# Kernel tuning notes

Hardware: AMD Instinct MI355X
Metric: run time of the kernel (lower is better)

The kernel has to match this reference:

```python
import jax, jax.numpy as jnp
import numpy as np

EPS = 1e-5  # matches repo calc_mean_std eps


def _mvn(x):
    # mean-variance normalization per (B, C) over spatial dims, unbiased var (torch default)
    B, C, H, W = x.shape
    xf = x.reshape(B, C, H * W)
    m = xf.mean(-1, keepdims=True)
    v = xf.var(-1, ddof=1, keepdims=True)
    return ((xf - m) / jnp.sqrt(v + EPS)).reshape(x.shape)


def _conv1x1(x, w, b):
    # 1x1 conv == per-pixel channel mixing
    return jnp.einsum('oc,bchw->bohw', w, x) + b[None, :, None, None]


def _content_sa(x, Wp, bp):
    B, C, H, W = x.shape
    n = H * W
    xn = _mvn(x)
    q = _conv1x1(xn, Wp[0], bp[0]).reshape(B, C, n)  # f
    k = _conv1x1(xn, Wp[1], bp[1]).reshape(B, C, n)  # g
    energy = jnp.einsum('bci,bcj->bij', q, k)        # [B, N, N]
    attn = jax.nn.softmax(energy, axis=-1)
    v = _conv1x1(x, Wp[2], bp[2]).reshape(B, C, n)   # h
    out = jnp.einsum('bcj,bij->bci', v, attn).reshape(B, C, H, W)
    return _conv1x1(out, Wp[3], bp[3]) + x


def _style_sa(x, Wp, bp):
    B, C, H, W = x.shape
    n = H * W
    f = _conv1x1(x, Wp[0], bp[0]).reshape(B, C, n)
    g = _conv1x1(x, Wp[1], bp[1]).reshape(B, C, n)
    energy = jnp.einsum('bci,bdi->bcd', f, g)        # [B, C, C] channel attention
    attn = jax.nn.softmax(energy, axis=-1)
    h = _conv1x1(_mvn(x), Wp[2], bp[2]).reshape(B, C, n)
    out = jnp.einsum('bdc,bdi->bci', attn, h).reshape(B, C, H, W)  # attn^T @ h
    return _conv1x1(out, Wp[3], bp[3]) + x


def _ca(c, s, Wp, bp):
    B, C, Hc, Wc = c.shape
    nc = Hc * Wc
    _, _, Hs, Ws = s.shape
    ns = Hs * Ws
    q = _conv1x1(_mvn(c), Wp[0], bp[0]).reshape(B, C, nc)
    k = _conv1x1(_mvn(s), Wp[1], bp[1]).reshape(B, C, ns)
    energy = jnp.einsum('bci,bcj->bij', q, k)        # [B, Nc, Ns]
    attn = jax.nn.softmax(energy, axis=-1)
    v = _conv1x1(s, Wp[2], bp[2]).reshape(B, C, ns)
    out = jnp.einsum('bcj,bij->bci', v, attn).reshape(B, C, Hc, Wc)
    return _conv1x1(out, Wp[3], bp[3]) + c


def setup_inputs() -> dict:
    key = jax.random.key(0)
    ks = jax.random.split(key, 8)
    B, C, H, W = 4, 512, 64, 64
    scale = 0.02
    return {
        'content_feat': jax.random.normal(ks[0], (B, C, H, W), jnp.float32),
        'style_feat': jax.random.normal(ks[1], (B, C, H, W), jnp.float32),
        'csa_w': jax.random.normal(ks[2], (4, C, C), jnp.float32) * scale,
        'csa_b': jnp.zeros((4, C), jnp.float32),
        'ssa_w': jax.random.normal(ks[3], (4, C, C), jnp.float32) * scale,
        'ssa_b': jnp.zeros((4, C), jnp.float32),
        'ca_w': jax.random.normal(ks[4], (4, C, C), jnp.float32) * scale,
        'ca_b': jnp.zeros((4, C), jnp.float32),
    }


def reference(content_feat, style_feat, csa_w, csa_b, ssa_w, ssa_b, ca_w, ca_b):
    cf = _content_sa(content_feat, csa_w, csa_b)
    sf = _style_sa(style_feat, ssa_w, ssa_b)
    return _ca(cf, sf, ca_w, ca_b)
```

## Files before the change

### kernel.cpp

```cpp
#include <hip/hip_runtime.h>
#include <math.h>


#define B_ 4
#define C_ 512
#define N_ 4096
#define TM 128
#define TN 128

typedef unsigned short u16;
typedef __attribute__((ext_vector_type(8))) short s8v;
typedef __attribute__((ext_vector_type(4))) float f4v;

__device__ __forceinline__ u16 f2bf(float x) {
  unsigned u = __float_as_uint(x);
  return (u16)((u + 0x7fffu + ((u >> 16) & 1u)) >> 16);
}
__device__ __forceinline__ float bf2f(u16 h) {
  return __uint_as_float(((unsigned)h) << 16);
}
__device__ __forceinline__ u16 f2h(float x) {
  union { _Float16 h; u16 u; } z;
  z.h = (_Float16)x;
  return z.u;
}
__device__ __forceinline__ float h2f(u16 v) {
  union { _Float16 h; u16 u; } z;
  z.u = v;
  return (float)z.h;
}

__device__ __forceinline__ void gload16(const void* g, void* l) {
  __builtin_amdgcn_global_load_lds(
      (const __attribute__((address_space(1))) unsigned int*)g,
      (__attribute__((address_space(3))) unsigned int*)l, 16, 0, 0);
}

__device__ __forceinline__ float wave_red_sum(float v) {
#pragma unroll
  for (int off = 32; off > 0; off >>= 1) v += __shfl_xor(v, off, 64);
  return v;
}
__device__ __forceinline__ float wave_red_max(float v) {
#pragma unroll
  for (int off = 32; off > 0; off >>= 1) v = fmaxf(v, __shfl_xor(v, off, 64));
  return v;
}

__global__ __launch_bounds__(256) void row_stats_k(const float* __restrict__ x,
                                                   float* __restrict__ mean,
                                                   float* __restrict__ rstd) {
  long row = blockIdx.x;
  const float* p = x + row * (long)N_;
  int t = threadIdx.x;
  float s = 0.f, ss = 0.f;
  for (int i = t * 4; i < N_; i += 1024) {
    float4 v = *(const float4*)(p + i);
    s += v.x + v.y + v.z + v.w;
    ss += v.x * v.x + v.y * v.y + v.z * v.z + v.w * v.w;
  }
  __shared__ float rs_[4], rss_[4];
  int wid = t >> 6, lane = t & 63;
  s = wave_red_sum(s);
  ss = wave_red_sum(ss);
  if (lane == 0) { rs_[wid] = s; rss_[wid] = ss; }
  __syncthreads();
  if (t == 0) {
    float S = rs_[0] + rs_[1] + rs_[2] + rs_[3];
    float SS = rss_[0] + rss_[1] + rss_[2] + rss_[3];
    float m = S / (float)N_;
    float var = (SS - (float)N_ * m * m) / (float)(N_ - 1);
    mean[row] = m;
    rstd[row] = rsqrtf(var + 1e-5f);
  }
}

__global__ __launch_bounds__(256) void row_stats_bf_k(
    const u16* __restrict__ x, float* __restrict__ mean,
    float* __restrict__ rstd) {
  long row = blockIdx.x;
  const u16* p = x + row * (long)N_;
  int t = threadIdx.x;
  float s = 0.f, ss = 0.f;
  for (int i = t * 8; i < N_; i += 2048) {
    ushort4 a = *(const ushort4*)(p + i);
    ushort4 b = *(const ushort4*)(p + i + 4);
    float v0 = bf2f(a.x), v1 = bf2f(a.y), v2 = bf2f(a.z), v3 = bf2f(a.w);
    float v4 = bf2f(b.x), v5 = bf2f(b.y), v6 = bf2f(b.z), v7 = bf2f(b.w);
    s += v0 + v1 + v2 + v3 + v4 + v5 + v6 + v7;
    ss += v0 * v0 + v1 * v1 + v2 * v2 + v3 * v3 + v4 * v4 + v5 * v5 +
          v6 * v6 + v7 * v7;
  }
  __shared__ float rs_[4], rss_[4];
  int wid = t >> 6, lane = t & 63;
  s = wave_red_sum(s);
  ss = wave_red_sum(ss);
  if (lane == 0) { rs_[wid] = s; rss_[wid] = ss; }
  __syncthreads();
  if (t == 0) {
    float S = rs_[0] + rs_[1] + rs_[2] + rs_[3];
    float SS = rss_[0] + rss_[1] + rss_[2] + rss_[3];
    float m = S / (float)N_;
    float var = (SS - (float)N_ * m * m) / (float)(N_ - 1);
    mean[row] = m;
    rstd[row] = rsqrtf(var + 1e-5f);
  }
}

__global__ __launch_bounds__(256) void cvt3_k(
    const float* __restrict__ a, const float* __restrict__ b,
    const float* __restrict__ c, u16* __restrict__ oa, u16* __restrict__ ob,
    u16* __restrict__ oc, long n) {
  const float* in = blockIdx.y == 0 ? a : (blockIdx.y == 1 ? b : c);
  u16* o = blockIdx.y == 0 ? oa : (blockIdx.y == 1 ? ob : oc);
  long i = ((long)blockIdx.x * 256 + threadIdx.x) * 4;
  if (i >= n) return;
  float4 v = *(const float4*)(in + i);
  *(ushort4*)(o + i) = make_ushort4(f2bf(v.x), f2bf(v.y), f2bf(v.z), f2bf(v.w));
}

template <bool HAS2, bool HAS3>
__global__ __launch_bounds__(256) void t_cvt_k(
    const float* __restrict__ X, const float* __restrict__ mean,
    const float* __restrict__ rstd, u16* __restrict__ o1,
    u16* __restrict__ o2, u16* __restrict__ o3) {
  __shared__ float tile[64][68];
  const int b = blockIdx.z;
  const int c0 = blockIdx.y * 64, i0 = blockIdx.x * 64;
  const int t = threadIdx.x;
  const int tr = t >> 4, tc = (t & 15) << 2;
  const long CN = (long)C_ * N_;
  const float* Xb = X + (long)b * CN;
#pragma unroll
  for (int p2 = 0; p2 < 4; ++p2) {
    int c = p2 * 16 + tr;
    float4 v = *(const float4*)(Xb + (long)(c0 + c) * N_ + i0 + tc);
    tile[c][tc] = v.x;
    tile[c][tc + 1] = v.y;
    tile[c][tc + 2] = v.z;
    tile[c][tc + 3] = v.w;
    if (HAS3) {
      *(ushort4*)(o3 + (long)b * CN + (long)(c0 + c) * N_ + i0 + tc) =
          make_ushort4(f2bf(v.x), f2bf(v.y), f2bf(v.z), f2bf(v.w));
    }
  }
  __syncthreads();
  float mv[4], rv[4];
#pragma unroll
  for (int j = 0; j < 4; ++j) {
    mv[j] = mean[b * C_ + c0 + tc + j];
    rv[j] = rstd[b * C_ + c0 + tc + j];
  }
#pragma unroll
  for (int p2 = 0; p2 < 4; ++p2) {
    int ir = p2 * 16 + tr;
    long off = (long)b * CN + (long)(i0 + ir) * C_ + c0 + tc;
    u16 h1[4], h2[4];
#pragma unroll
    for (int j = 0; j < 4; ++j) {
      float v = tile[tc + j][ir];
      if (HAS2) h2[j] = f2bf(v);
      h1[j] = f2bf((v - mv[j]) * rv[j]);
    }
    *(ushort4*)(o1 + off) = make_ushort4(h1[0], h1[1], h1[2], h1[3]);
    if (HAS2) *(ushort4*)(o2 + off) = make_ushort4(h2[0], h2[1], h2[2], h2[3]);
  }
}

template <bool HAS2>
__global__ __launch_bounds__(256) void t_cvt_bf_k(
    const u16* __restrict__ X, const float* __restrict__ mean,
    const float* __restrict__ rstd, u16* __restrict__ o1,
    u16* __restrict__ o2) {
  __shared__ float tile[64][68];
  const int b = blockIdx.z;
  const int c0 = blockIdx.y * 64, i0 = blockIdx.x * 64;
  const int t = threadIdx.x;
  const int tr = t >> 4, tc = (t & 15) << 2;
  const long CN = (long)C_ * N_;
  const u16* Xb = X + (long)b * CN;
#pragma unroll
  for (int p2 = 0; p2 < 4; ++p2) {
    int c = p2 * 16 + tr;
    ushort4 v = *(const ushort4*)(Xb + (long)(c0 + c) * N_ + i0 + tc);
    tile[c][tc] = bf2f(v.x);
    tile[c][tc + 1] = bf2f(v.y);
    tile[c][tc + 2] = bf2f(v.z);
    tile[c][tc + 3] = bf2f(v.w);
  }
  __syncthreads();
  float mv[4], rv[4];
#pragma unroll
  for (int j = 0; j < 4; ++j) {
    mv[j] = mean[b * C_ + c0 + tc + j];
    rv[j] = rstd[b * C_ + c0 + tc + j];
  }
#pragma unroll
  for (int p2 = 0; p2 < 4; ++p2) {
    int ir = p2 * 16 + tr;
    long off = (long)b * CN + (long)(i0 + ir) * C_ + c0 + tc;
    u16 h1[4], h2[4];
#pragma unroll
    for (int j = 0; j < 4; ++j) {
      float v = tile[tc + j][ir];
      if (HAS2) h2[j] = f2bf(v);
      h1[j] = f2bf((v - mv[j]) * rv[j]);
    }
    *(ushort4*)(o1 + off) = make_ushort4(h1[0], h1[1], h1[2], h1[3]);
    if (HAS2) *(ushort4*)(o2 + off) = make_ushort4(h2[0], h2[1], h2[2], h2[3]);
  }
}

__global__ __launch_bounds__(256) void softmax_bf_k(const u16* __restrict__ E,
                                                    u16* __restrict__ ph) {
  long row = blockIdx.x;
  const u16* p = E + row * (long)N_;
  int t = threadIdx.x;
  float v[16];
  float mx = -3.4e38f;
#pragma unroll
  for (int q = 0; q < 4; ++q) {
    ushort4 w4 = *(const ushort4*)(p + t * 16 + q * 4);
    v[q * 4 + 0] = h2f(w4.x);
    v[q * 4 + 1] = h2f(w4.y);
    v[q * 4 + 2] = h2f(w4.z);
    v[q * 4 + 3] = h2f(w4.w);
    mx = fmaxf(mx, fmaxf(fmaxf(v[q * 4], v[q * 4 + 1]),
                         fmaxf(v[q * 4 + 2], v[q * 4 + 3])));
  }
  __shared__ float red[4];
  int wid = t >> 6, lane = t & 63;
  mx = wave_red_max(mx);
  if (lane == 0) red[wid] = mx;
  __syncthreads();
  mx = fmaxf(fmaxf(red[0], red[1]), fmaxf(red[2], red[3]));
  float s = 0.f;
#pragma unroll
  for (int i = 0; i < 16; ++i) {
    v[i] = __expf(v[i] - mx);
    s += v[i];
  }
  __syncthreads();
  s = wave_red_sum(s);
  if (lane == 0) red[wid] = s;
  __syncthreads();
  s = red[0] + red[1] + red[2] + red[3];
  float inv = 1.f / s;
  long ob = row * (long)N_ + t * 16;
#pragma unroll
  for (int q = 0; q < 4; ++q) {
    *(ushort4*)(ph + ob + q * 4) =
        make_ushort4(f2bf(v[q * 4 + 0] * inv), f2bf(v[q * 4 + 1] * inv),
                     f2bf(v[q * 4 + 2] * inv), f2bf(v[q * 4 + 3] * inv));
  }
}

__global__ __launch_bounds__(256) void softmax_t_k(const float* __restrict__ E2,
                                                   u16* __restrict__ ph) {
  int b = blockIdx.x >> 9;
  int x = blockIdx.x & 511;
  const float* p = E2 + ((long)b * C_ + x) * C_;
  int t = threadIdx.x;
  float v0 = p[t * 2], v1 = p[t * 2 + 1];
  float mx = fmaxf(v0, v1);
  __shared__ float red[4];
  int wid = t >> 6, lane = t & 63;
  mx = wave_red_max(mx);
  if (lane == 0) red[wid] = mx;
  __syncthreads();
  mx = fmaxf(fmaxf(red[0], red[1]), fmaxf(red[2], red[3]));
  v0 = __expf(v0 - mx);
  v1 = __expf(v1 - mx);
  float s = v0 + v1;
  __syncthreads();
  s = wave_red_sum(s);
  if (lane == 0) red[wid] = s;
  __syncthreads();
  s = red[0] + red[1] + red[2] + red[3];
  float inv = 1.f / s;
  long base = (long)b * C_ * C_;
  ph[base + (long)(t * 2) * C_ + x] = f2bf(v0 * inv);
  ph[base + (long)(t * 2 + 1) * C_ + x] = f2bf(v1 * inv);
}

__global__ __launch_bounds__(256) void redk_k(const float* __restrict__ P,
                                              long pKS, long perB, int nsplit,
                                              float* __restrict__ of,
                                              long total) {
  long e = ((long)blockIdx.x * 256 + threadIdx.x) * 4;
  if (e >= total) return;
  long b = e / perB, rem = e - b * perB;
  const float* p0 = P + b * perB + rem;
  float4 s = *(const float4*)p0;
  for (int k = 1; k < nsplit; ++k) {
    float4 t = *(const float4*)(p0 + (long)k * pKS);
    s.x += t.x;
    s.y += t.y;
    s.z += t.z;
    s.w += t.w;
  }
  *(float4*)(of + b * perB + rem) = s;
}

template <int OUTM, int BIAS, int RESM, bool SWAP>
__global__ __launch_bounds__(256, 3) void mm_k(
    const u16* __restrict__ Ap, long aBS, int lda,
    const u16* __restrict__ Bp, long bBS, int ldb,
    float* Of, u16* __restrict__ Obf, long oBS, long oKS, int ldo,
    const float* __restrict__ bias, const float* resp,
    const u16* __restrict__ res16, long rBS, int K, int nsplit) {
  __shared__ u16 lds[16384];
  const int bxi = SWAP ? blockIdx.y : blockIdx.x;
  const int byi = SWAP ? blockIdx.x : blockIdx.y;
  const int b = blockIdx.z / nsplit;
  const int ks = blockIdx.z % nsplit;
  const int Kc = K / nsplit;
  const int k0beg = ks * Kc;
  const int m0 = byi * TM, n0 = bxi * TN;
  const int t = threadIdx.x, lane = t & 63, wid = t >> 6;
  const int wm = (wid >> 1) * 64, wn = (wid & 1) * 64;

  const u16* srcp = (wid < 2) ? (Ap + (long)b * aBS) : (Bp + (long)b * bBS);
  const int sld = (wid < 2) ? lda : ldb;
  const long srow0 = ((wid < 2) ? m0 : n0) + (wid & 1) * 64;
  u16* dstb = &lds[wid * 4096];
  const int srg = lane >> 3;
  const int ssl = lane & 7;

  f4v acc[4][4];
#pragma unroll
  for (int i = 0; i < 4; ++i)
#pragma unroll
    for (int j = 0; j < 4; ++j) acc[i][j] = (f4v){0.f, 0.f, 0.f, 0.f};

  const int lr = lane & 15, ksl = lane >> 4;
  const u16* lA = &lds[0];
  const u16* lB = &lds[8192];

  for (int k0 = k0beg; k0 < k0beg + Kc; k0 += 64) {
#pragma unroll
    for (int s = 0; s < 8; ++s) {
      int r = s * 8 + srg;
      int kb = ((ssl ^ (r & 7)) << 4);
      const u16* gp = srcp + (srow0 + r) * (long)sld + k0;
      gload16((const char*)gp + kb, dstb + s * 512);
    }
    __syncthreads();
#pragma unroll
    for (int kk = 0; kk < 2; ++kk) {
      s8v ar[4], br[4];
#pragma unroll
      for (int f = 0; f < 4; ++f) {
        int ra = wm + f * 16 + lr;
        ar[f] = *(const s8v*)(lA + ra * 64 +
                              ((((kk << 2) | ksl) ^ (ra & 7)) << 3));
        int rb = wn + f * 16 + lr;
        br[f] = *(const s8v*)(lB + rb * 64 +
                              ((((kk << 2) | ksl) ^ (rb & 7)) << 3));
      }
#pragma unroll
      for (int i = 0; i < 4; ++i)
#pragma unroll
        for (int j = 0; j < 4; ++j)
          acc[i][j] = __builtin_amdgcn_mfma_f32_16x16x32_bf16(
              ar[i], br[j], acc[i][j], 0, 0, 0);
    }
    __syncthreads();
  }

  const float* resb = (RESM == 1) ? (resp + (long)b * rBS) : nullptr;
  const u16* resb16 = (RESM == 2) ? (res16 + (long)b * rBS) : nullptr;
  long obase = (long)b * oBS + (long)ks * oKS;
#pragma unroll
  for (int i = 0; i < 4; ++i) {
#pragma unroll
    for (int j = 0; j < 4; ++j) {
#pragma unroll
      for (int e = 0; e < 4; ++e) {
        int m = m0 + wm + i * 16 + ksl * 4 + e;
        int n = n0 + wn + j * 16 + lr;
        float v = acc[i][j][e];
        if (BIAS == 1) v += bias[m];
        if (BIAS == 2) v += bias[n];
        if (RESM == 1) v += resb[(long)m * ldo + n];
        if (RESM == 2) v += bf2f(resb16[(long)m * ldo + n]);
        long o = obase + (long)m * ldo + n;
        if (OUTM == 0) {
          Of[o] = v;
        } else if (OUTM == 1) {
          Obf[o] = f2bf(v);
        } else {
          Obf[o] = f2h(v);
        }
      }
    }
  }
}

extern "C" void kernel_launch(void* const* d_in, const int* in_sizes, int n_in,
                              void* d_out, int out_size, void* d_ws,
                              size_t ws_size, hipStream_t stream) {
  (void)in_sizes; (void)n_in; (void)out_size;
  const long CN = (long)C_ * N_;
  const long CC = (long)C_ * C_;

  const float* xc = (const float*)d_in[0];
  const float* xs = (const float*)d_in[1];
  const float* cw = (const float*)d_in[2];
  const float* cb = (const float*)d_in[3];
  const float* sw = (const float*)d_in[4];
  const float* sb = (const float*)d_in[5];
  const float* aw = (const float*)d_in[6];
  const float* ab = (const float*)d_in[7];
  float* out = (float*)d_out;

  char* w = (char*)d_ws;
  auto carve = [&](size_t bytes) {
    char* r = w;
    w += (bytes + 255) & ~(size_t)255;
    return r;
  };
  u16* cwb = (u16*)carve(4 * CC * 2);
  u16* swb = (u16*)carve(4 * CC * 2);
  u16* awb = (u16*)carve(4 * CC * 2);
  float* stats = (float*)carve(8 * B_ * C_ * 4);
  float* m1 = stats, *r1 = m1 + B_ * C_, *m2 = r1 + B_ * C_, *r2 = m2 + B_ * C_;
  float* m3 = r2 + B_ * C_, *r3 = m3 + B_ * C_, *m4 = r3 + B_ * C_,
       *r4 = m4 + B_ * C_;
  float* E2buf = (float*)carve(B_ * CC * 4);
  u16* aT = (u16*)carve(B_ * CC * 2);
  const size_t SLOT = (size_t)B_ * CN * 4;
  char* s0 = carve(SLOT);
  char* s1 = carve(SLOT);
  char* s2 = carve(SLOT);
  char* s3 = carve(SLOT);
  u16* xcb = (u16*)carve(B_ * CN * 2);
  u16* xsb = (u16*)carve(B_ * CN * 2);
  size_t used = (size_t)(w - (char*)d_ws);
  int S = N_;
  while (S > 128 && used + (size_t)4 * B_ * S * N_ > ws_size) S >>= 1;
  u16* E16 = (u16*)carve((size_t)B_ * S * N_ * 2);
  u16* AT = (u16*)carve((size_t)B_ * S * N_ * 2);
  float* EregF = (float*)E16;

  u16* sA = (u16*)s0;
  u16* sB = (u16*)s1;
  u16* sC = (u16*)s2;
  u16* sD = (u16*)s3;
  u16* at0 = AT;
  u16* at1 = AT + B_ * CN;
  u16* at2 = AT + 2 * B_ * CN;

  const int e2s = 8;

  dim3 blk(256);
  dim3 gQ(4, 32, B_);
  dim3 gVs(4, 32, B_);
  dim3 gQK(8, 32, B_);
  dim3 gFGs(8, 32, B_);
  dim3 gTs(N_ / 64, C_ / 64, B_);

  cvt3_k<<<dim3(1024, 3), blk, 0, stream>>>(cw, sw, aw, cwb, swb, awb, 4 * CC);

  auto attention = [&](const u16* Qp, int ldq, long qBS, const u16* Kp,
                       int ldk, long kBS, const u16* Vp, u16* oT) {
    for (int i0 = 0; i0 < N_; i0 += S) {
      mm_k<2, 0, 0, false><<<dim3(N_ / TN, S / TM, B_), blk, 0, stream>>>(
          Qp + (long)i0 * ldq, qBS, ldq, Kp, kBS, ldk, nullptr, E16,
          (long)S * N_, 0, N_, nullptr, nullptr, nullptr, 0, C_, 1);
      softmax_bf_k<<<B_ * S, blk, 0, stream>>>(E16, AT);
      mm_k<1, 0, 0, false><<<dim3(C_ / TN, S / TM, B_), blk, 0, stream>>>(
          AT, (long)S * N_, N_, Vp, CN, N_, nullptr, oT + (long)i0 * C_, CN,
          0, C_, nullptr, nullptr, nullptr, 0, N_, 1);
    }
  };

  row_stats_k<<<B_ * C_, blk, 0, stream>>>(xc, m1, r1);
  row_stats_k<<<B_ * C_, blk, 0, stream>>>(xs, m2, r2);
  t_cvt_k<true, true><<<gTs, blk, 0, stream>>>(xc, m1, r1, sA, sB, xcb);
  mm_k<1, 2, 0, false><<<gQK, blk, 0, stream>>>(sA, CN, C_, cwb, 0, C_,
      nullptr, sC, (long)N_ * 1024, 0, 1024, cb, nullptr, nullptr, 0, C_, 1);
  mm_k<1, 1, 0, true><<<gVs, blk, 0, stream>>>(cwb + 2 * CC, 0, C_, sB, CN,
      C_, nullptr, sD, CN, 0, N_, cb + 2 * C_, nullptr, nullptr, 0, C_, 1);
  attention(sC, 1024, (long)N_ * 1024, sC + 512, 1024, (long)N_ * 1024, sD,
            sA);
  mm_k<1, 1, 2, true><<<gVs, blk, 0, stream>>>(cwb + 3 * CC, 0, C_, sA, CN,
      C_, nullptr, sB, CN, 0, N_, cb + 3 * C_, nullptr, xcb, CN, C_, 1);

  t_cvt_k<true, true><<<gTs, blk, 0, stream>>>(xs, m2, r2, sA, sC, xsb);
  mm_k<1, 1, 0, true><<<gFGs, blk, 0, stream>>>(swb, 0, C_, sC, CN, C_,
      nullptr, sD, (long)1024 * N_, 0, N_, sb, nullptr, nullptr, 0, C_, 1);
  mm_k<1, 2, 0, false><<<gQ, blk, 0, stream>>>(sA, CN, C_, swb + 2 * CC, 0,
      C_, nullptr, at0, CN, 0, C_, sb + 2 * C_, nullptr, nullptr, 0, C_, 1);
  mm_k<0, 0, 0, false><<<dim3(4, 4, B_ * e2s), blk, 0, stream>>>(
      sD, (long)1024 * N_, N_, sD + (long)512 * N_, (long)1024 * N_, N_,
      EregF, nullptr, CC, (long)B_ * CC, C_, nullptr, nullptr, nullptr, 0, N_,
      e2s);
  redk_k<<<(B_ * (int)CC) / 1024, blk, 0, stream>>>(
      EregF, (long)B_ * CC, CC, e2s, E2buf, (long)B_ * CC);
  softmax_t_k<<<B_ * C_, blk, 0, stream>>>(E2buf, aT);
  mm_k<1, 0, 0, false><<<gQ, blk, 0, stream>>>(at0, CN, C_, aT, CC, C_,
      nullptr, sA, CN, 0, C_, nullptr, nullptr, nullptr, 0, C_, 1);
  mm_k<1, 1, 2, true><<<gVs, blk, 0, stream>>>(swb + 3 * CC, 0, C_, sA, CN,
      C_, nullptr, sC, CN, 0, N_, sb + 3 * C_, nullptr, xsb, CN, C_, 1);

  row_stats_bf_k<<<B_ * C_, blk, 0, stream>>>(sB, m3, r3);
  row_stats_bf_k<<<B_ * C_, blk, 0, stream>>>(sC, m4, r4);
  t_cvt_bf_k<false><<<gTs, blk, 0, stream>>>(sB, m3, r3, at0, nullptr);
  t_cvt_bf_k<true><<<gTs, blk, 0, stream>>>(sC, m4, r4, at1, at2);
  mm_k<1, 2, 0, false><<<gQ, blk, 0, stream>>>(at0, CN, C_, awb, 0, C_,
      nullptr, sD, CN, 0, C_, ab, nullptr, nullptr, 0, C_, 1);
  mm_k<1, 2, 0, false><<<gQ, blk, 0, stream>>>(at1, CN, C_, awb + CC, 0, C_,
      nullptr, sA, CN, 0, C_, ab + C_, nullptr, nullptr, 0, C_, 1);
  mm_k<1, 1, 0, true><<<gVs, blk, 0, stream>>>(awb + 2 * CC, 0, C_, at2, CN,
      C_, nullptr, sC, CN, 0, N_, ab + 2 * C_, nullptr, nullptr, 0, C_, 1);
  attention(sD, C_, CN, sA, C_, CN, sC, sD);
  mm_k<0, 1, 2, true><<<gVs, blk, 0, stream>>>(awb + 3 * CC, 0, C_, sD, CN,
      C_, out, nullptr, CN, 0, N_, ab + 3 * C_, nullptr, sB, CN, C_, 1);
}
```

Before: 1.111 ms.

## Fuse softmax into PV matmul with online-softmax rescaling

Replaces the separate softmax kernel and P@V matmul with one kernel that reads fp16 energy tiles, computes a running max/sum softmax per row on the fly, converts probabilities to bf16, and feeds them straight into MFMA against V. This removes the write and re-read of the full normalized attention matrix and one launch per chunk. In exchange, each of the C/TN column blocks recomputes exp over the same energy rows, and every k-step adds rescaling and cross-lane shuffle work.

```diff
diff --git a/kernel.cpp b/kernel.cpp
--- a/kernel.cpp
+++ b/kernel.cpp
@@ -208,50 +208,6 @@
     }
     *(ushort4*)(o1 + off) = make_ushort4(h1[0], h1[1], h1[2], h1[3]);
     if (HAS2) *(ushort4*)(o2 + off) = make_ushort4(h2[0], h2[1], h2[2], h2[3]);
-  }
-}
-
-__global__ __launch_bounds__(256) void softmax_bf_k(const u16* __restrict__ E,
-                                                    u16* __restrict__ ph) {
-  long row = blockIdx.x;
-  const u16* p = E + row * (long)N_;
-  int t = threadIdx.x;
-  float v[16];
-  float mx = -3.4e38f;
-#pragma unroll
-  for (int q = 0; q < 4; ++q) {
-    ushort4 w4 = *(const ushort4*)(p + t * 16 + q * 4);
-    v[q * 4 + 0] = h2f(w4.x);
-    v[q * 4 + 1] = h2f(w4.y);
-    v[q * 4 + 2] = h2f(w4.z);
-    v[q * 4 + 3] = h2f(w4.w);
-    mx = fmaxf(mx, fmaxf(fmaxf(v[q * 4], v[q * 4 + 1]),
-                         fmaxf(v[q * 4 + 2], v[q * 4 + 3])));
-  }
-  __shared__ float red[4];
-  int wid = t >> 6, lane = t & 63;
-  mx = wave_red_max(mx);
-  if (lane == 0) red[wid] = mx;
-  __syncthreads();
-  mx = fmaxf(fmaxf(red[0], red[1]), fmaxf(red[2], red[3]));
-  float s = 0.f;
-#pragma unroll
-  for (int i = 0; i < 16; ++i) {
-    v[i] = __expf(v[i] - mx);
-    s += v[i];
-  }
-  __syncthreads();
-  s = wave_red_sum(s);
-  if (lane == 0) red[wid] = s;
-  __syncthreads();
-  s = red[0] + red[1] + red[2] + red[3];
-  float inv = 1.f / s;
-  long ob = row * (long)N_ + t * 16;
-#pragma unroll
-  for (int q = 0; q < 4; ++q) {
-    *(ushort4*)(ph + ob + q * 4) =
-        make_ushort4(f2bf(v[q * 4 + 0] * inv), f2bf(v[q * 4 + 1] * inv),
-                     f2bf(v[q * 4 + 2] * inv), f2bf(v[q * 4 + 3] * inv));
   }
 }
 
@@ -392,6 +348,123 @@
         } else {
           Obf[o] = f2h(v);
         }
+      }
+    }
+  }
+}
+
+__global__ __launch_bounds__(256, 2) void pv_fused_k(
+    const u16* __restrict__ Ep, long eBS, const u16* __restrict__ Vp,
+    long vBS, u16* __restrict__ Obf, long oBS) {
+  __shared__ u16 lds[16384];
+  const int b = blockIdx.z;
+  const int m0 = blockIdx.y * TM, n0 = blockIdx.x * TN;
+  const int t = threadIdx.x, lane = t & 63, wid = t >> 6;
+  const int wm = (wid >> 1) * 64, wn = (wid & 1) * 64;
+
+  const u16* srcp = (wid < 2) ? (Ep + (long)b * eBS) : (Vp + (long)b * vBS);
+  const long srow0 = ((wid < 2) ? m0 : n0) + (wid & 1) * 64;
+  u16* dstb = &lds[wid * 4096];
+  const int srg = lane >> 3, ssl = lane & 7;
+  const int lr = lane & 15, ksl = lane >> 4;
+  const u16* lA = &lds[0];
+  const u16* lB = &lds[8192];
+
+  f4v acc[4][4];
+#pragma unroll
+  for (int i = 0; i < 4; ++i)
+#pragma unroll
+    for (int j = 0; j < 4; ++j) acc[i][j] = (f4v){0.f, 0.f, 0.f, 0.f};
+  float run_m[4] = {-3.4e38f, -3.4e38f, -3.4e38f, -3.4e38f};
+  float run_l[4] = {0.f, 0.f, 0.f, 0.f};
+
+  for (int k0 = 0; k0 < N_; k0 += 64) {
+#pragma unroll
+    for (int s = 0; s < 8; ++s) {
+      int r = s * 8 + srg;
+      int kb = ((ssl ^ (r & 7)) << 4);
+      const u16* gp = srcp + (srow0 + r) * (long)N_ + k0;
+      gload16((const char*)gp + kb, dstb + s * 512);
+    }
+    __syncthreads();
+
+    s8v pf[4][2];
+    float sc[4];
+#pragma unroll
+    for (int f = 0; f < 4; ++f) {
+      int ra = wm + f * 16 + lr;
+      float v[16];
+#pragma unroll
+      for (int kk = 0; kk < 2; ++kk) {
+        s8v raw = *(const s8v*)(lA + ra * 64 +
+                                ((((kk << 2) | ksl) ^ (ra & 7)) << 3));
+#pragma unroll
+        for (int j2 = 0; j2 < 8; ++j2) v[kk * 8 + j2] = h2f((u16)raw[j2]);
+      }
+      float mx = v[0];
+#pragma unroll
+      for (int q = 1; q < 16; ++q) mx = fmaxf(mx, v[q]);
+      mx = fmaxf(mx, __shfl_xor(mx, 16, 64));
+      mx = fmaxf(mx, __shfl_xor(mx, 32, 64));
+      float nm = fmaxf(run_m[f], mx);
+      sc[f] = __expf(run_m[f] - nm);
+      run_m[f] = nm;
+      float s2 = 0.f;
+#pragma unroll
+      for (int q = 0; q < 16; ++q) {
+        v[q] = __expf(v[q] - nm);
+        s2 += v[q];
+      }
+      s2 += __shfl_xor(s2, 16, 64);
+      s2 += __shfl_xor(s2, 32, 64);
+      run_l[f] = run_l[f] * sc[f] + s2;
+#pragma unroll
+      for (int kk = 0; kk < 2; ++kk) {
+        s8v p;
+#pragma unroll
+        for (int j2 = 0; j2 < 8; ++j2) p[j2] = (short)f2bf(v[kk * 8 + j2]);
+        pf[f][kk] = p;
+      }
+    }
+#pragma unroll
+    for (int i = 0; i < 4; ++i) {
+#pragma unroll
+      for (int e = 0; e < 4; ++e) {
+        float se = __shfl(sc[i], ksl * 4 + e, 64);
+#pragma unroll
+        for (int j = 0; j < 4; ++j) acc[i][j][e] *= se;
+      }
+    }
+#pragma unroll
+    for (int kk = 0; kk < 2; ++kk) {
+      s8v br[4];
+#pragma unroll
+      for (int f = 0; f < 4; ++f) {
+        int rb = wn + f * 16 + lr;
+        br[f] = *(const s8v*)(lB + rb * 64 +
+                              ((((kk << 2) | ksl) ^ (rb & 7)) << 3));
+      }
+#pragma unroll
+      for (int i = 0; i < 4; ++i)
+#pragma unroll
+        for (int j = 0; j < 4; ++j)
+          acc[i][j] = __builtin_amdgcn_mfma_f32_16x16x32_bf16(
+              pf[i][kk], br[j], acc[i][j], 0, 0, 0);
+    }
+    __syncthreads();
+  }
+
+#pragma unroll
+  for (int i = 0; i < 4; ++i) {
+#pragma unroll
+    for (int e = 0; e < 4; ++e) {
+      float le = __shfl(run_l[i], ksl * 4 + e, 64);
+      float inv = 1.f / le;
+      int m = m0 + wm + i * 16 + ksl * 4 + e;
+#pragma unroll
+      for (int j = 0; j < 4; ++j) {
+        int n = n0 + wn + j * 16 + lr;
+        Obf[(long)b * oBS + (long)m * C_ + n] = f2bf(acc[i][j][e] * inv);
       }
     }
   }
@@ -468,10 +541,8 @@
       mm_k<2, 0, 0, false><<<dim3(N_ / TN, S / TM, B_), blk, 0, stream>>>(
           Qp + (long)i0 * ldq, qBS, ldq, Kp, kBS, ldk, nullptr, E16,
           (long)S * N_, 0, N_, nullptr, nullptr, nullptr, 0, C_, 1);
-      softmax_bf_k<<<B_ * S, blk, 0, stream>>>(E16, AT);
-      mm_k<1, 0, 0, false><<<dim3(C_ / TN, S / TM, B_), blk, 0, stream>>>(
-          AT, (long)S * N_, N_, Vp, CN, N_, nullptr, oT + (long)i0 * C_, CN,
-          0, C_, nullptr, nullptr, nullptr, 0, N_, 1);
+      pv_fused_k<<<dim3(C_ / TN, S / TM, B_), blk, 0, stream>>>(
+          E16, (long)S * N_, Vp, CN, oT + (long)i0 * C_, CN);
     }
   };
 
```

Measured after the change: 1.785 ms. 60.6% more time.
